# Kernel tuning notes

Measured on AMD Instinct MI355X. Metric: run time of the kernel, lower is better.

The kernel has to match this reference:

```python
import jax, jax.numpy as jnp
import numpy as np

H = 256
L = 5
N = 50000


def setup_inputs() -> dict:
    key = jax.random.key(0)
    ks = jax.random.split(key, 12)
    E = 800000
    x = jax.random.normal(ks[0], (N, H), dtype=jnp.float32)
    edge_index = jax.random.randint(ks[1], (2, E), 0, N, dtype=jnp.int64)
    edge_weight = jax.random.uniform(ks[2], (E,), dtype=jnp.float32)
    s = 1.0 / np.sqrt(H)
    weight = jax.random.uniform(ks[3], (L, H, H), dtype=jnp.float32, minval=-s, maxval=s)
    w_ih = jax.random.uniform(ks[4], (3 * H, H), dtype=jnp.float32, minval=-s, maxval=s)
    w_hh = jax.random.uniform(ks[5], (3 * H, H), dtype=jnp.float32, minval=-s, maxval=s)
    b_ih = jax.random.uniform(ks[6], (3 * H,), dtype=jnp.float32, minval=-s, maxval=s)
    b_hh = jax.random.uniform(ks[7], (3 * H,), dtype=jnp.float32, minval=-s, maxval=s)
    fc_w = jax.random.uniform(ks[8], (1, H), dtype=jnp.float32, minval=-s, maxval=s)
    fc_b = jax.random.uniform(ks[9], (1,), dtype=jnp.float32, minval=-s, maxval=s)
    return {"x": x, "edge_index": edge_index, "edge_weight": edge_weight,
            "weight": weight, "w_ih": w_ih, "w_hh": w_hh, "b_ih": b_ih,
            "b_hh": b_hh, "fc_w": fc_w, "fc_b": fc_b, "prob": 0}


def _gru_cell(m, h, w_ih, w_hh, b_ih, b_hh):
    # PyTorch GRUCell: gates ordered (r, z, n)
    gi = m @ w_ih.T + b_ih  # [N, 3H]
    gh = h @ w_hh.T + b_hh  # [N, 3H]
    r = jax.nn.sigmoid(gi[:, :H] + gh[:, :H])
    z = jax.nn.sigmoid(gi[:, H:2 * H] + gh[:, H:2 * H])
    n = jnp.tanh(gi[:, 2 * H:] + r * gh[:, 2 * H:])
    return (1.0 - z) * n + z * h


def reference(x, edge_index, edge_weight, weight, w_ih, w_hh, b_ih, b_hh, fc_w, fc_b, prob):
    src = edge_index[0]
    dst = edge_index[1]
    h = x
    for i in range(L):
        m = h @ weight[i]                       # [N, H] per-layer linear transform
        msg = edge_weight[:, None] * m[src]     # [E, H] gather + edge weighting
        agg = jax.ops.segment_sum(msg, dst, num_segments=N)  # scatter-add
        h = _gru_cell(agg, h, w_ih, w_hh, b_ih, b_hh)
    h = jax.nn.relu(h)
    # dropout with p=prob; reference runs deterministically with p=0 (eval mode)
    out = h @ fc_w.T + fc_b                     # [N, 1]
    return out
```

## Files before the change

kernel.cpp:

```cpp
#include <hip/hip_runtime.h>
#include <hip/hip_bf16.h>
#include <math.h>


#define HDIM 256

using bf16x8 = __attribute__((ext_vector_type(8))) short;
using f32x4  = __attribute__((ext_vector_type(4))) float;

__device__ __forceinline__ bf16x8 ldfrag(const ushort* p) {
    union { uint4 u; bf16x8 f; } x;
    x.u = *(const uint4*)p;
    return x.f;
}
#define MFMA(a, b, c) __builtin_amdgcn_mfma_f32_16x16x32_bf16((a), (b), (c), 0, 0, 0)
#define GLD16(g, l)                                                            \
    __builtin_amdgcn_global_load_lds(                                          \
        (const __attribute__((address_space(1))) void*)(g),                    \
        (__attribute__((address_space(3))) void*)(l), 16, 0, 0)

__device__ __forceinline__ float ldf(const void* p, size_t i, int isbf) {
    if (isbf) return __bfloat162float(((const __hip_bfloat16*)p)[i]);
    return ((const float*)p)[i];
}
__device__ __forceinline__ ushort f2bs(float v) {
    __hip_bfloat16 b = __float2bfloat16(v);
    return *(ushort*)&b;
}
__device__ __forceinline__ float bs2f(ushort u) {
    __hip_bfloat16 b = *(__hip_bfloat16*)&u;
    return __bfloat162float(b);
}
__device__ __forceinline__ float unpk(uint u) {
    return __uint_as_float(u << 16) + __uint_as_float(u & 0xffff0000u);
}
__device__ __forceinline__ uint pk(float v) {
    const ushort hi = f2bs(v);
    const ushort lo = f2bs(v - bs2f(hi));
    return (uint)hi | ((uint)lo << 16);
}
__device__ __forceinline__ size_t taddrH(int n, int k) {
    return (size_t)(n >> 4) * 4096 + (size_t)((k >> 5) << 9)
         + (size_t)(((k >> 3) & 3) << 7) + (size_t)((n & 15) << 3) + (k & 7);
}
__device__ __forceinline__ size_t taddrA(int n, int k) {
    return (size_t)(n >> 4) * 8192 + (size_t)((k >> 5) << 9)
         + (size_t)(((k >> 3) & 3) << 7) + (size_t)((n & 15) << 3) + (k & 7);
}

__global__ void detect_k(const void* x, const void* ei, int* flags) {
    if (blockIdx.x == 0 && threadIdx.x == 0) {
        const __hip_bfloat16* xb = (const __hip_bfloat16*)x;
        int isbf = 1;
        for (int i = 0; i < 1024; ++i) {
            float v = fabsf(__bfloat162float(xb[i]));
            if (!(v < 1e6f)) { isbf = 0; break; }
        }
        flags[0] = isbf;
        const int* e32 = (const int*)ei;
        int orv = e32[1] | e32[3] | e32[5] | e32[7] | e32[9] | e32[11];
        flags[1] = (orv == 0) ? 1 : 0;
    }
}

__global__ void conv_h0_k(const void* x, ushort* HH, ushort* HL, uint* hlin,
                          const int* flags, int useHL, int Nn, size_t npad256) {
    size_t i = (size_t)blockIdx.x * blockDim.x + threadIdx.x;
    if (i >= npad256) return;
    const int n = (int)(i >> 8), k = (int)(i & 255);
    float v = 0.f;
    if (n < Nn) v = ldf(x, i, flags[0]);
    const ushort hi = f2bs(v);
    const size_t a = taddrH(n, k);
    HH[a] = hi;
    if (useHL) HL[a] = f2bs(v - bs2f(hi));
    hlin[i] = (uint)hi | ((uint)f2bs(v - bs2f(hi)) << 16);
}

__global__ __launch_bounds__(256)
void prep1_k(const void* wih, const void* w, float* wihp, const int* flags) {
    __shared__ float As[16][260], Bs[16][260];
    const int bx = blockIdx.x;
    const int l = bx / 768, rem = bx % 768;
    const int rt = (rem >> 4) << 4, kt = (rem & 15) << 4;
    const int tid = threadIdx.x, isbf = flags[0];
    for (int idx = tid; idx < 4096; idx += 256) {
        const int row = idx >> 8, col = idx & 255;
        As[row][col] = ldf(wih, (size_t)(rt + row) * 256 + col, isbf);
        Bs[row][col] = ldf(w, (size_t)l * 65536 + (size_t)(kt + row) * 256 + col, isbf);
    }
    __syncthreads();
    const int ri = tid >> 4, ki = tid & 15;
    float acc = 0.f;
    for (int j = 0; j < 256; ++j) acc = fmaf(As[ri][j], Bs[ki][j], acc);
    wihp[((size_t)l * 768 + rt + ri) * 256 + kt + ki] = acc;
}

__global__ void prep2_k(const float* __restrict__ wihp, const void* whh,
                        const void* bih, const void* bhh,
                        ushort* BgAH, ushort* BgAL, ushort* BgBH, ushort* BgBL,
                        float* bsum, float* bni, float* bnh,
                        const int* flags, int L) {
    const int i = blockIdx.x * blockDim.x + threadIdx.x;
    const int isbf = flags[0];
    if (i < (L << 19)) {
        const int l = i >> 19, r2 = i & 524287;
        const int j = r2 >> 9, k = r2 & 511;
        const int g = (j >> 4) & 3, b = ((j >> 6) << 4) + (j & 15);
        const int kk = k & 255;
        const float v = (g == 3) ? 0.f
                      : wihp[((size_t)l * 768 + g * 256 + b) * 256 + kk];
        const ushort hi = f2bs(v);
        const int ct = j >> 4, c = k >> 5;
        const size_t a = (size_t)l * 524288 + (size_t)(ct * 16 + c) * 512
                       + (size_t)(((k >> 3) & 3) << 7) + ((j & 15) << 3) + (k & 7);
        BgAH[a] = hi; BgAL[a] = f2bs(v - bs2f(hi));
    }
    if (i < 524288) {
        const int j = i >> 9, k = i & 511;
        const int g = (j >> 4) & 3, b = ((j >> 6) << 4) + (j & 15);
        const int kk = k & 255;
        float v;
        if (g == 0)      v = ldf(whh, (size_t)b * 256 + kk, isbf);
        else if (g == 1) v = ldf(whh, (size_t)(256 + b) * 256 + kk, isbf);
        else if (g == 2) v = 0.f;
        else             v = ldf(whh, (size_t)(512 + b) * 256 + kk, isbf);
        const ushort hi = f2bs(v);
        const int ct = j >> 4, c = k >> 5;
        const size_t a = (size_t)(ct * 16 + c) * 512
                       + (size_t)(((k >> 3) & 3) << 7) + ((j & 15) << 3) + (k & 7);
        BgBH[a] = hi; BgBL[a] = f2bs(v - bs2f(hi));
    }
    if (i < 512) bsum[i] = ldf(bih, i, isbf) + ldf(bhh, i, isbf);
    if (i < 256) {
        bni[i] = ldf(bih, 512 + i, isbf);
        bnh[i] = ldf(bhh, 512 + i, isbf);
    }
}


__global__ void zero_int_k(int* p, int n) {
    int i = blockIdx.x * blockDim.x + threadIdx.x;
    if (i < n) p[i] = 0;
}

__global__ void count_k(const void* ei, int* cnt, const int* flags, int E) {
    int e = blockIdx.x * blockDim.x + threadIdx.x;
    if (e >= E) return;
    const int* e32 = (const int*)ei;
    int d = flags[1] ? e32[2 * ((size_t)E + e)] : e32[(size_t)E + e];
    atomicAdd(&cnt[d], 1);
}

__global__ __launch_bounds__(256)
void scan1_k(const int* cnt, int* ptr, int* bsumN, int N) {
    __shared__ int s[256];
    const int t = threadIdx.x;
    const int gid = blockIdx.x * 256 + t;
    int v = (gid < N) ? cnt[gid] : 0;
    const int own = v;
    s[t] = v;
    __syncthreads();
#pragma unroll
    for (int off = 1; off < 256; off <<= 1) {
        int add = (t >= off) ? s[t - off] : 0;
        __syncthreads();
        s[t] += add;
        __syncthreads();
    }
    if (gid < N) ptr[gid] = s[t] - own;
    if (t == 255) bsumN[blockIdx.x] = s[255];
}

__global__ __launch_bounds__(256)
void scan2_k(int* bsumN, int NB) {
    __shared__ int s[256];
    __shared__ int carry;
    const int t = threadIdx.x;
    if (t == 0) carry = 0;
    __syncthreads();
    for (int base = 0; base < NB; base += 256) {
        const int i = base + t;
        int v = (i < NB) ? bsumN[i] : 0;
        const int own = v;
        s[t] = v;
        __syncthreads();
#pragma unroll
        for (int off = 1; off < 256; off <<= 1) {
            int add = (t >= off) ? s[t - off] : 0;
            __syncthreads();
            s[t] += add;
            __syncthreads();
        }
        if (i < NB) bsumN[i] = carry + s[t] - own;
        __syncthreads();
        if (t == 0) carry += s[255];
        __syncthreads();
    }
}

__global__ void scan3_k(int* ptr, int* cursor, const int* bsumN, int N, int E) {
    const int gid = blockIdx.x * 256 + threadIdx.x;
    if (gid < N) {
        const int p = ptr[gid] + bsumN[blockIdx.x];
        ptr[gid] = p;
        cursor[gid] = p;
    }
    if (gid == 0) ptr[N] = E;
}

__global__ void fill_k(const void* ei, const void* ew, int* cursor,
                       int* srcs, float* wse, const int* flags, int E) {
    int e = blockIdx.x * blockDim.x + threadIdx.x;
    if (e >= E) return;
    const int* e32 = (const int*)ei;
    int s, d;
    if (flags[1]) { s = e32[2 * (size_t)e]; d = e32[2 * ((size_t)E + e)]; }
    else          { s = e32[e];             d = e32[(size_t)E + e]; }
    const int p = atomicAdd(&cursor[d], 1);
    srcs[p] = s;
    wse[p] = ldf(ew, e, flags[0]);
}

__global__ __launch_bounds__(256)
void spmm_k(const uint* __restrict__ hlin, const int* __restrict__ ptr,
            const int* __restrict__ srcs, const float* __restrict__ wse,
            ushort* __restrict__ AGG, int N) {
    const int node = blockIdx.x * 4 + (threadIdx.x >> 6);
    if (node >= N) return;
    const int lane = threadIdx.x & 63;
    const int lane4 = lane << 2;
    const uint4* hl = (const uint4*)hlin;
    const int p0 = ptr[node], p1 = ptr[node + 1];
    float4 acc = make_float4(0.f, 0.f, 0.f, 0.f);
    int j = p0;
    for (; j + 1 < p1; j += 2) {
        const int s0 = srcs[j], s1 = srcs[j + 1];
        const float w0 = wse[j], w1 = wse[j + 1];
        const uint4 u0 = hl[(size_t)s0 * 64 + lane];
        const uint4 u1 = hl[(size_t)s1 * 64 + lane];
        acc.x = fmaf(w0, unpk(u0.x), acc.x); acc.y = fmaf(w0, unpk(u0.y), acc.y);
        acc.z = fmaf(w0, unpk(u0.z), acc.z); acc.w = fmaf(w0, unpk(u0.w), acc.w);
        acc.x = fmaf(w1, unpk(u1.x), acc.x); acc.y = fmaf(w1, unpk(u1.y), acc.y);
        acc.z = fmaf(w1, unpk(u1.z), acc.z); acc.w = fmaf(w1, unpk(u1.w), acc.w);
    }
    if (j < p1) {
        const int s0 = srcs[j];
        const float w0 = wse[j];
        const uint4 u0 = hl[(size_t)s0 * 64 + lane];
        acc.x = fmaf(w0, unpk(u0.x), acc.x); acc.y = fmaf(w0, unpk(u0.y), acc.y);
        acc.z = fmaf(w0, unpk(u0.z), acc.z); acc.w = fmaf(w0, unpk(u0.w), acc.w);
    }
    ushort4 hi, lo;
    hi.x = f2bs(acc.x); lo.x = f2bs(acc.x - bs2f(hi.x));
    hi.y = f2bs(acc.y); lo.y = f2bs(acc.y - bs2f(hi.y));
    hi.z = f2bs(acc.z); lo.z = f2bs(acc.z - bs2f(hi.z));
    hi.w = f2bs(acc.w); lo.w = f2bs(acc.w - bs2f(hi.w));
    *(ushort4*)&AGG[taddrA(node, lane4)] = hi;
    *(ushort4*)&AGG[taddrA(node, 256 + lane4)] = lo;
}

__global__ __launch_bounds__(256)
void gates_k(const ushort* __restrict__ AGG,
             const ushort* __restrict__ HH, const ushort* __restrict__ HL,
             const ushort* __restrict__ BgAH, const ushort* __restrict__ BgAL,
             const ushort* __restrict__ BgBH, const ushort* __restrict__ BgBL,
             const float* __restrict__ bsum, const float* __restrict__ bni,
             const float* __restrict__ bnh,
             ushort* __restrict__ HnH, ushort* __restrict__ HnL,
             uint* __restrict__ hlin,
             const int* __restrict__ flags, int useHL, int nRB) {
    __shared__ ushort lds[24576];
    const int x = blockIdx.x & 7, rem = blockIdx.x >> 3;
    const int cgB = rem & 7, rbHi = rem >> 3;
    const int rb = rbHi * 8 + x;
    if (rb >= nRB) return;
    const int tid = threadIdx.x, lane = tid & 63;
    const int wv = __builtin_amdgcn_readfirstlane(tid >> 6);
    const int wr = wv & 1, wc = wv >> 1;
    const int lm = lane & 15, lq = lane >> 4;
    const int fullsplit = !flags[0];
    const int rt = rb * 8, t0 = 2 * wv;
    f32x4 acc[4][4];
#pragma unroll
    for (int i = 0; i < 4; ++i)
#pragma unroll
        for (int j = 0; j < 4; ++j) acc[i][j] = (f32x4){0.f, 0.f, 0.f, 0.f};

#define GT_STEP(BH, BL, c0l, A0, ASTRIDE, JSKIP, DOLO)                         \
    do {                                                                       \
        __syncthreads();                                                       \
        GLD16((A0) + (size_t)lane * 8, &lds[t0 * 512]);                        \
        GLD16((A0) + (ASTRIDE) + (size_t)lane * 8, &lds[t0 * 512 + 512]);      \
        GLD16((A0) + 512 + (size_t)lane * 8, &lds[12288 + t0 * 512]);          \
        GLD16((A0) + (ASTRIDE) + 512 + (size_t)lane * 8, &lds[12288 + t0 * 512 + 512]); \
        const size_t bb = ((size_t)(8 * cgB + t0) * 16 + (size_t)(c0l)) * 512; \
        if ((t0 & 3) != (JSKIP)) {                                             \
            GLD16((BH) + bb + (size_t)lane * 8, &lds[4096 + t0 * 512]);        \
            GLD16((BH) + bb + 512 + (size_t)lane * 8, &lds[12288 + 4096 + t0 * 512]); \
        }                                                                      \
        if (((t0 + 1) & 3) != (JSKIP)) {                                       \
            GLD16((BH) + bb + 8192 + (size_t)lane * 8, &lds[4096 + t0 * 512 + 512]); \
            GLD16((BH) + bb + 8704 + (size_t)lane * 8, &lds[12288 + 4096 + t0 * 512 + 512]); \
        }                                                                      \
        if (DOLO) {                                                            \
            if ((t0 & 3) != (JSKIP)) {                                         \
                GLD16((BL) + bb + (size_t)lane * 8, &lds[8192 + t0 * 512]);    \
                GLD16((BL) + bb + 512 + (size_t)lane * 8, &lds[12288 + 8192 + t0 * 512]); \
            }                                                                  \
            if (((t0 + 1) & 3) != (JSKIP)) {                                   \
                GLD16((BL) + bb + 8192 + (size_t)lane * 8, &lds[8192 + t0 * 512 + 512]); \
                GLD16((BL) + bb + 8704 + (size_t)lane * 8, &lds[12288 + 8192 + t0 * 512 + 512]); \
            }                                                                  \
        }                                                                      \
        __syncthreads();                                                       \
        _Pragma("unroll")                                                      \
        for (int sb = 0; sb < 2; ++sb) {                                       \
            const int lb = sb * 12288;                                         \
            bf16x8 af[4];                                                      \
            _Pragma("unroll")                                                  \
            for (int i = 0; i < 4; ++i)                                        \
                af[i] = ldfrag(&lds[lb + (4 * wr + i) * 512 + lq * 128 + lm * 8]); \
            _Pragma("unroll")                                                  \
            for (int j = 0; j < 4; ++j) {                                      \
                if (j == (JSKIP)) continue;                                    \
                const bf16x8 bj = ldfrag(&lds[lb + 4096 + (4 * wc + j) * 512 + lq * 128 + lm * 8]); \
                _Pragma("unroll")                                              \
                for (int i = 0; i < 4; ++i) acc[i][j] = MFMA(af[i], bj, acc[i][j]); \
            }                                                                  \
            if (DOLO) {                                                        \
                _Pragma("unroll")                                              \
                for (int j = 0; j < 4; ++j) {                                  \
                    if (j == (JSKIP)) continue;                                \
                    const bf16x8 bl = ldfrag(&lds[lb + 8192 + (4 * wc + j) * 512 + lq * 128 + lm * 8]); \
                    _Pragma("unroll")                                          \
                    for (int i = 0; i < 4; ++i) acc[i][j] = MFMA(af[i], bl, acc[i][j]); \
                }                                                              \
            }                                                                  \
        }                                                                      \
    } while (0)

    for (int s = 0; s < 4; ++s) {
        const ushort* a0 = AGG + (size_t)(rt + t0) * 8192 + (size_t)(2 * s) * 512;
        GT_STEP(BgAH, BgAL, 2 * s, a0, 8192, 3, fullsplit);
    }
    for (int s = 4; s < 8; ++s) {
        const ushort* a0 = AGG + (size_t)(rt + t0) * 8192 + (size_t)(2 * s) * 512;
        GT_STEP(BgAH, BgAL, 2 * s, a0, 8192, 3, 0);
    }
    for (int s = 8; s < 12; ++s) {
        const ushort* a0 = HH + (size_t)(rt + t0) * 4096 + (size_t)(2 * s - 16) * 512;
        GT_STEP(BgBH, BgBL, 2 * s - 16, a0, 4096, 2, fullsplit);
    }
    if (useHL) {
        for (int s = 12; s < 16; ++s) {
            const ushort* a0 = HL + (size_t)(rt + t0) * 4096 + (size_t)(2 * s - 24) * 512;
            GT_STEP(BgBH, BgBL, 2 * s - 16, a0, 4096, 2, 0);
        }
    }
#undef GT_STEP

    const int b = (2 * cgB + wc) * 16 + lm;
    const float rbias = bsum[b], zbias = bsum[256 + b];
    const float ibias = bni[b], hbias = bnh[b];
#pragma unroll
    for (int i = 0; i < 4; ++i) {
        const int row0 = rb * 128 + wr * 64 + i * 16 + lq * 4;
#pragma unroll
        for (int v = 0; v < 4; ++v) {
            const int row = row0 + v;
            const size_t ho = taddrH(row, b);
            float hold = bs2f(HH[ho]);
            if (useHL) hold += bs2f(HL[ho]);
            const float r = 1.f / (1.f + expf(-(acc[i][0][v] + rbias)));
            const float z = 1.f / (1.f + expf(-(acc[i][1][v] + zbias)));
            const float nn = tanhf(acc[i][2][v] + ibias + r * (acc[i][3][v] + hbias));
            const float hv = (1.f - z) * nn + z * hold;
            const ushort hi = f2bs(hv);
            HnH[ho] = hi;
            if (useHL) HnL[ho] = f2bs(hv - bs2f(hi));
            hlin[(size_t)row * 256 + b] = (uint)hi | ((uint)f2bs(hv - bs2f(hi)) << 16);
        }
    }
}

__global__ void final_k(const ushort* __restrict__ HH, const ushort* __restrict__ HL,
                        const void* fcw, const void* fcb,
                        void* out, const int* flags, int useHL, int N) {
    const int n = blockIdx.x;
    const int t = threadIdx.x;
    const int isbf = flags[0];
    const size_t off = taddrH(n, t);
    float h = bs2f(HH[off]);
    if (useHL) h += bs2f(HL[off]);
    float v = fmaxf(h, 0.f) * ldf(fcw, t, isbf);
#pragma unroll
    for (int offx = 32; offx >= 1; offx >>= 1) v += __shfl_down(v, offx);
    __shared__ float red[4];
    if ((t & 63) == 0) red[t >> 6] = v;
    __syncthreads();
    if (t == 0) {
        const float s = red[0] + red[1] + red[2] + red[3] + ldf(fcb, 0, isbf);
        if (isbf) ((__hip_bfloat16*)out)[n] = __float2bfloat16(s);
        else      ((float*)out)[n] = s;
    }
}

extern "C" void kernel_launch(void* const* d_in, const int* in_sizes, int n_in,
                              void* d_out, int out_size, void* d_ws, size_t ws_size,
                              hipStream_t stream) {
    const int H = HDIM;
    const int N = in_sizes[0] / H;
    const int E = in_sizes[2];
    const int L = in_sizes[3] / (H * H);
    const int NB = (N + 255) / 256;
    const int nRB = (N + 127) / 128;
    const size_t NPAD = (size_t)nRB * 128;
    const size_t hHalf = NPAD * 256;
    const size_t aggHalf = NPAD * 512;

    char* p = (char*)d_ws;
    int*    flags = (int*)p;              p += 64;
    ushort* AGG  = (ushort*)p;            p += aggHalf * 2;
    ushort* HxH  = (ushort*)p;            p += hHalf * 2;
    ushort* HyH  = (ushort*)p;            p += hHalf * 2;
    uint*   hlin = (uint*)p;              p += NPAD * 256 * 4;
    float*  wihp = (float*)p;             p += (size_t)L * 768 * 256 * 4;
    ushort* BgAH = (ushort*)p;            p += (size_t)L * 524288 * 2;
    ushort* BgAL = (ushort*)p;            p += (size_t)L * 524288 * 2;
    ushort* BgBH = (ushort*)p;            p += (size_t)524288 * 2;
    ushort* BgBL = (ushort*)p;            p += (size_t)524288 * 2;
    float*  bsum = (float*)p;             p += 512 * 4;
    float*  bni  = (float*)p;             p += 256 * 4;
    float*  bnh  = (float*)p;             p += 256 * 4;
    int*    ptr  = (int*)p;               p += (size_t)(N + 1) * 4;
    int*    cursor = (int*)p;             p += (size_t)N * 4;
    int*    bsumN  = (int*)p;             p += (size_t)NB * 4;
    int*    srcs   = (int*)p;             p += (size_t)E * 4;
    float*  wse    = (float*)p;           p += (size_t)E * 4;
    const size_t need_reduced = (size_t)(p - (char*)d_ws);
    ushort* HxL = (ushort*)p;
    ushort* HyL = (ushort*)(p + hHalf * 2);
    const size_t need_full = need_reduced + 2 * hHalf * 2;
    const int useHL = (ws_size >= need_full) ? 1 : 0;
    if (!useHL) { HxL = HxH; HyL = HyH; }

    detect_k<<<dim3(1), dim3(64), 0, stream>>>(d_in[0], d_in[1], flags);
    conv_h0_k<<<dim3((unsigned)NPAD), dim3(256), 0, stream>>>(
        d_in[0], HxH, HxL, hlin, flags, useHL, N, NPAD * 256);
    prep1_k<<<dim3((unsigned)(L * 768)), dim3(256), 0, stream>>>(
        d_in[4], d_in[3], wihp, flags);
    prep2_k<<<dim3((unsigned)(L * 2048)), dim3(256), 0, stream>>>(
        wihp, d_in[5], d_in[6], d_in[7],
        BgAH, BgAL, BgBH, BgBL, bsum, bni, bnh, flags, L);

    zero_int_k<<<dim3(NB), dim3(256), 0, stream>>>(cursor, N);
    count_k<<<dim3((E + 255) / 256), dim3(256), 0, stream>>>(d_in[1], cursor, flags, E);
    scan1_k<<<dim3(NB), dim3(256), 0, stream>>>(cursor, ptr, bsumN, N);
    scan2_k<<<dim3(1), dim3(256), 0, stream>>>(bsumN, NB);
    scan3_k<<<dim3(NB), dim3(256), 0, stream>>>(ptr, cursor, bsumN, N, E);
    fill_k<<<dim3((E + 255) / 256), dim3(256), 0, stream>>>(
        d_in[1], d_in[2], cursor, srcs, wse, flags, E);

    const dim3 blk(256);
    const unsigned gGrid = 64u * (unsigned)((nRB + 7) / 8);
    ushort *HcH = HxH, *HcL = HxL, *HnH = HyH, *HnL = HyL;
    for (int l = 0; l < L; ++l) {
        spmm_k<<<dim3((N + 3) / 4), blk, 0, stream>>>(hlin, ptr, srcs, wse, AGG, N);
        gates_k<<<dim3(gGrid), blk, 0, stream>>>(
            AGG, HcH, HcL,
            BgAH + (size_t)l * 524288, BgAL + (size_t)l * 524288,
            BgBH, BgBL, bsum, bni, bnh, HnH, HnL, hlin, flags, useHL, nRB);
        ushort* t;
        t = HcH; HcH = HnH; HnH = t;
        t = HcL; HcL = HnL; HnL = t;
    }
    final_k<<<dim3(N), blk, 0, stream>>>(
        HcH, HcL, d_in[8], d_in[9], d_out, flags, useHL, N);
}
```

Baseline: 1.884 ms.

## Store hidden state as split hi/lo bf16 rows and repack after gates

Replaces the interleaved hi|lo packed hidden buffer with a row layout holding a 256-wide hi half followed by a 256-wide lo half. The gates kernel no longer writes this row-major copy with scattered 4-byte stores; a new repack kernel copies the tiled HnH/HnL buffers into it with 16-byte loads and stores. In the SpMM, each lane reads 8 bf16 values per edge: lanes 0-31 cover the hi half and lanes 32-63 the lo half, and the two halves are summed with a cross-lane xor shuffle before vectorised 16-byte AGG stores. This aims for coalesced stores and cheaper unpacking, at the cost of one extra kernel launch and an extra full pass over the hidden state per layer.

```diff
diff --git a/kernel.cpp b/kernel.cpp
--- a/kernel.cpp
+++ b/kernel.cpp
@@ -30,14 +30,6 @@
 __device__ __forceinline__ float bs2f(ushort u) {
     __hip_bfloat16 b = *(__hip_bfloat16*)&u;
     return __bfloat162float(b);
-}
-__device__ __forceinline__ float unpk(uint u) {
-    return __uint_as_float(u << 16) + __uint_as_float(u & 0xffff0000u);
-}
-__device__ __forceinline__ uint pk(float v) {
-    const ushort hi = f2bs(v);
-    const ushort lo = f2bs(v - bs2f(hi));
-    return (uint)hi | ((uint)lo << 16);
 }
 __device__ __forceinline__ size_t taddrH(int n, int k) {
     return (size_t)(n >> 4) * 4096 + (size_t)((k >> 5) << 9)
@@ -63,7 +55,7 @@
     }
 }
 
-__global__ void conv_h0_k(const void* x, ushort* HH, ushort* HL, uint* hlin,
+__global__ void conv_h0_k(const void* x, ushort* HH, ushort* HL, ushort* hB,
                           const int* flags, int useHL, int Nn, size_t npad256) {
     size_t i = (size_t)blockIdx.x * blockDim.x + threadIdx.x;
     if (i >= npad256) return;
@@ -71,10 +63,27 @@
     float v = 0.f;
     if (n < Nn) v = ldf(x, i, flags[0]);
     const ushort hi = f2bs(v);
+    const ushort lo = f2bs(v - bs2f(hi));
     const size_t a = taddrH(n, k);
     HH[a] = hi;
-    if (useHL) HL[a] = f2bs(v - bs2f(hi));
-    hlin[i] = (uint)hi | ((uint)f2bs(v - bs2f(hi)) << 16);
+    if (useHL) HL[a] = lo;
+    hB[(size_t)n * 512 + k] = hi;
+    hB[(size_t)n * 512 + 256 + k] = lo;
+}
+
+__global__ void repack_k(const ushort* __restrict__ TH, const ushort* __restrict__ TL,
+                         ushort* __restrict__ hB, int useHL, int ngroups) {
+    const int g = blockIdx.x * 256 + threadIdx.x;
+    if (g >= ngroups) return;
+    const int t = g >> 9, o = (g & 511) * 8;
+    const int k = ((o >> 9) << 5) | (((o >> 7) & 3) << 3);
+    const int n = t * 16 + ((o >> 3) & 15);
+    const uint4 hv = *(const uint4*)&TH[(size_t)t * 4096 + o];
+    *(uint4*)&hB[(size_t)n * 512 + k] = hv;
+    uint4 lv;
+    if (useHL) lv = *(const uint4*)&TL[(size_t)t * 4096 + o];
+    else       lv = make_uint4(0u, 0u, 0u, 0u);
+    *(uint4*)&hB[(size_t)n * 512 + 256 + k] = lv;
 }
 
 __global__ __launch_bounds__(256)
@@ -223,41 +232,51 @@
 }
 
 __global__ __launch_bounds__(256)
-void spmm_k(const uint* __restrict__ hlin, const int* __restrict__ ptr,
+void spmm_k(const ushort* __restrict__ hB, const int* __restrict__ ptr,
             const int* __restrict__ srcs, const float* __restrict__ wse,
             ushort* __restrict__ AGG, int N) {
     const int node = blockIdx.x * 4 + (threadIdx.x >> 6);
     if (node >= N) return;
     const int lane = threadIdx.x & 63;
-    const int lane4 = lane << 2;
-    const uint4* hl = (const uint4*)hlin;
     const int p0 = ptr[node], p1 = ptr[node + 1];
-    float4 acc = make_float4(0.f, 0.f, 0.f, 0.f);
+    float av[8];
+#pragma unroll
+    for (int i = 0; i < 8; ++i) av[i] = 0.f;
+    union U8 { ushort u[8]; uint4 v; };
     int j = p0;
     for (; j + 1 < p1; j += 2) {
         const int s0 = srcs[j], s1 = srcs[j + 1];
         const float w0 = wse[j], w1 = wse[j + 1];
-        const uint4 u0 = hl[(size_t)s0 * 64 + lane];
-        const uint4 u1 = hl[(size_t)s1 * 64 + lane];
-        acc.x = fmaf(w0, unpk(u0.x), acc.x); acc.y = fmaf(w0, unpk(u0.y), acc.y);
-        acc.z = fmaf(w0, unpk(u0.z), acc.z); acc.w = fmaf(w0, unpk(u0.w), acc.w);
-        acc.x = fmaf(w1, unpk(u1.x), acc.x); acc.y = fmaf(w1, unpk(u1.y), acc.y);
-        acc.z = fmaf(w1, unpk(u1.z), acc.z); acc.w = fmaf(w1, unpk(u1.w), acc.w);
+        U8 u0, u1;
+        u0.v = *(const uint4*)&hB[(size_t)s0 * 512 + lane * 8];
+        u1.v = *(const uint4*)&hB[(size_t)s1 * 512 + lane * 8];
+#pragma unroll
+        for (int i = 0; i < 8; ++i) av[i] = fmaf(w0, bs2f(u0.u[i]), av[i]);
+#pragma unroll
+        for (int i = 0; i < 8; ++i) av[i] = fmaf(w1, bs2f(u1.u[i]), av[i]);
     }
     if (j < p1) {
         const int s0 = srcs[j];
         const float w0 = wse[j];
-        const uint4 u0 = hl[(size_t)s0 * 64 + lane];
-        acc.x = fmaf(w0, unpk(u0.x), acc.x); acc.y = fmaf(w0, unpk(u0.y), acc.y);
-        acc.z = fmaf(w0, unpk(u0.z), acc.z); acc.w = fmaf(w0, unpk(u0.w), acc.w);
-    }
-    ushort4 hi, lo;
-    hi.x = f2bs(acc.x); lo.x = f2bs(acc.x - bs2f(hi.x));
-    hi.y = f2bs(acc.y); lo.y = f2bs(acc.y - bs2f(hi.y));
-    hi.z = f2bs(acc.z); lo.z = f2bs(acc.z - bs2f(hi.z));
-    hi.w = f2bs(acc.w); lo.w = f2bs(acc.w - bs2f(hi.w));
-    *(ushort4*)&AGG[taddrA(node, lane4)] = hi;
-    *(ushort4*)&AGG[taddrA(node, 256 + lane4)] = lo;
+        U8 u0;
+        u0.v = *(const uint4*)&hB[(size_t)s0 * 512 + lane * 8];
+#pragma unroll
+        for (int i = 0; i < 8; ++i) av[i] = fmaf(w0, bs2f(u0.u[i]), av[i]);
+    }
+#pragma unroll
+    for (int i = 0; i < 8; ++i) av[i] += __shfl_xor(av[i], 32);
+    if (lane < 32) {
+        const int k0 = lane * 8;
+        union U8 hi8, lo8;
+#pragma unroll
+        for (int i = 0; i < 8; ++i) {
+            const ushort hi = f2bs(av[i]);
+            hi8.u[i] = hi;
+            lo8.u[i] = f2bs(av[i] - bs2f(hi));
+        }
+        *(uint4*)&AGG[taddrA(node, k0)] = hi8.v;
+        *(uint4*)&AGG[taddrA(node, 256 + k0)] = lo8.v;
+    }
 }
 
 __global__ __launch_bounds__(256)
@@ -268,7 +287,6 @@
              const float* __restrict__ bsum, const float* __restrict__ bni,
              const float* __restrict__ bnh,
              ushort* __restrict__ HnH, ushort* __restrict__ HnL,
-             uint* __restrict__ hlin,
              const int* __restrict__ flags, int useHL, int nRB) {
     __shared__ ushort lds[24576];
     const int x = blockIdx.x & 7, rem = blockIdx.x >> 3;
@@ -379,7 +397,6 @@
             const ushort hi = f2bs(hv);
             HnH[ho] = hi;
             if (useHL) HnL[ho] = f2bs(hv - bs2f(hi));
-            hlin[(size_t)row * 256 + b] = (uint)hi | ((uint)f2bs(hv - bs2f(hi)) << 16);
         }
     }
 }
@@ -424,7 +441,7 @@
     ushort* AGG  = (ushort*)p;            p += aggHalf * 2;
     ushort* HxH  = (ushort*)p;            p += hHalf * 2;
     ushort* HyH  = (ushort*)p;            p += hHalf * 2;
-    uint*   hlin = (uint*)p;              p += NPAD * 256 * 4;
+    ushort* hB   = (ushort*)p;            p += NPAD * 512 * 2;
     float*  wihp = (float*)p;             p += (size_t)L * 768 * 256 * 4;
     ushort* BgAH = (ushort*)p;            p += (size_t)L * 524288 * 2;
     ushort* BgAL = (ushort*)p;            p += (size_t)L * 524288 * 2;
@@ -447,7 +464,7 @@
 
     detect_k<<<dim3(1), dim3(64), 0, stream>>>(d_in[0], d_in[1], flags);
     conv_h0_k<<<dim3((unsigned)NPAD), dim3(256), 0, stream>>>(
-        d_in[0], HxH, HxL, hlin, flags, useHL, N, NPAD * 256);
+        d_in[0], HxH, HxL, hB, flags, useHL, N, NPAD * 256);
     prep1_k<<<dim3((unsigned)(L * 768)), dim3(256), 0, stream>>>(
         d_in[4], d_in[3], wihp, flags);
     prep2_k<<<dim3((unsigned)(L * 2048)), dim3(256), 0, stream>>>(
@@ -464,13 +481,17 @@
 
     const dim3 blk(256);
     const unsigned gGrid = 64u * (unsigned)((nRB + 7) / 8);
+    const int ngroups = (int)(NPAD * 32);
+    const unsigned rGrid = (unsigned)((ngroups + 255) / 256);
     ushort *HcH = HxH, *HcL = HxL, *HnH = HyH, *HnL = HyL;
     for (int l = 0; l < L; ++l) {
-        spmm_k<<<dim3((N + 3) / 4), blk, 0, stream>>>(hlin, ptr, srcs, wse, AGG, N);
+        spmm_k<<<dim3((N + 3) / 4), blk, 0, stream>>>(hB, ptr, srcs, wse, AGG, N);
         gates_k<<<dim3(gGrid), blk, 0, stream>>>(
             AGG, HcH, HcL,
             BgAH + (size_t)l * 524288, BgAL + (size_t)l * 524288,
-            BgBH, BgBL, bsum, bni, bnh, HnH, HnL, hlin, flags, useHL, nRB);
+            BgBH, BgBL, bsum, bni, bnh, HnH, HnL, flags, useHL, nRB);
+        if (l + 1 < L)
+            repack_k<<<dim3(rGrid), blk, 0, stream>>>(HnH, HnL, hB, useHL, ngroups);
         ushort* t;
         t = HcH; HcH = HnH; HnH = t;
         t = HcL; HcL = HnL; HnL = t;
```

New measurement: 1.962 ms. 4.2% more time.
